# Performance work log

Measured on AMD Instinct MI355X. Metric: run time of the kernel, lower is better.

## Reference

```python
import math
import jax, jax.numpy as jnp
import numpy as np

D_MODEL = 768
D_CROSS = 768
D_HEAD = 64
N_HEADS = D_MODEL // D_HEAD  # 12
D_FF = D_MODEL * 3           # 2304
EPS = 1e-6
N_FREQ = D_HEAD // 8         # freqs per axis (3 axes -> theta dim 24, rotates first 48 of 64 dims)


def make_rope_freqs():
    # k-diffusion style geometric frequencies in [pi, 10*pi), one table shared per head
    n = N_HEADS * N_FREQ
    f = np.exp(np.linspace(math.log(math.pi), math.log(10.0 * math.pi), n + 1)[:-1])
    return jnp.asarray(f.reshape(N_FREQ, N_HEADS).T, dtype=jnp.float32)  # [nh, N_FREQ]

ROPE_FREQS = make_rope_freqs()


def rms_norm(x, scale):
    ms = jnp.mean(jnp.square(x), axis=-1, keepdims=True)
    return x * (scale * jax.lax.rsqrt(ms + EPS))


def cos_scale(q, k, scale):
    # cosine-sim QK rescale: unit-normalize q,k per head then multiply by sqrt(learned scale)
    s = jnp.sqrt(scale)[:, None, None]  # [nh,1,1]
    q = q * (s * jax.lax.rsqrt(jnp.sum(jnp.square(q), -1, keepdims=True) + EPS))
    k = k * (s * jax.lax.rsqrt(jnp.sum(jnp.square(k), -1, keepdims=True) + EPS))
    return q, k


def rope_theta(pos):
    # pos [b,l,3] -> theta [b,nh,l,3*N_FREQ]
    b, l, _ = pos.shape
    th = pos[..., None, :, None] * ROPE_FREQS[:, None, :]  # [b,l,nh,3,N_FREQ]
    th = th.reshape(b, l, N_HEADS, 3 * N_FREQ)
    return jnp.swapaxes(th, 1, 2)  # movedim(-2,-3)


def apply_rope(x, theta):
    d = theta.shape[-1]
    x1, x2, x3 = x[..., :d], x[..., d:2 * d], x[..., 2 * d:]
    c, s = jnp.cos(theta), jnp.sin(theta)
    return jnp.concatenate([x1 * c - x2 * s, x2 * c + x1 * s, x3], axis=-1)


def sdpa(q, k, v):
    # scale=1.0 (cosine-sim already scaled)
    a = jax.nn.softmax(jnp.einsum('bhqe,bhke->bhqk', q, k), axis=-1)
    return jnp.einsum('bhqk,bhke->bhqe', a, v)


def reference(x, pos, x_cross, pos_cross,
              sa_norm_scale, sa_wqkv, sa_scale, sa_wout,
              ca_norm_scale, ca_norm_cross_scale, ca_wq, ca_wkv, ca_scale, ca_wout,
              ff_norm_scale, ff_wup, ff_wdown):
    b, l, _ = x.shape
    lc = x_cross.shape[1]

    # --- self attention ---
    h = rms_norm(x, sa_norm_scale)
    qkv = (h @ sa_wqkv.T).reshape(b, l, 3, N_HEADS, D_HEAD).transpose(2, 0, 3, 1, 4)
    q, k, v = qkv[0], qkv[1], qkv[2]  # [b,nh,l,e]
    q, k = cos_scale(q, k, sa_scale)
    theta = rope_theta(pos)
    q = apply_rope(q, theta)
    k = apply_rope(k, theta)
    o = sdpa(q, k, v)
    o = jnp.swapaxes(o, 1, 2).reshape(b, l, D_MODEL)
    x = o @ sa_wout.T + x

    # --- cross attention ---
    h = rms_norm(x, ca_norm_scale)
    hc = rms_norm(x_cross, ca_norm_cross_scale)
    q = (h @ ca_wq.T).reshape(b, l, N_HEADS, D_HEAD).transpose(0, 2, 1, 3)
    kv = (hc @ ca_wkv.T).reshape(b, lc, 2, N_HEADS, D_HEAD).transpose(2, 0, 3, 1, 4)
    k, v = kv[0], kv[1]
    q, k = cos_scale(q, k, ca_scale)
    q = apply_rope(q, rope_theta(pos))
    k = apply_rope(k, rope_theta(pos_cross))
    o = sdpa(q, k, v)
    o = jnp.swapaxes(o, 1, 2).reshape(b, l, D_MODEL)
    x = o @ ca_wout.T + x

    # --- SwiGLU FFN ---
    u = rms_norm(x, ff_norm_scale) @ ff_wup.T  # [b,l,2*d_ff]
    a, g = jnp.split(u, 2, axis=-1)
    x = (a * jax.nn.silu(g)) @ ff_wdown.T + x
    return x


def setup_inputs() -> dict:
    key = jax.random.key(0)
    ks = jax.random.split(key, 16)
    B, L = 2, 2048

    def w(k, out_f, in_f):
        return jax.random.normal(k, (out_f, in_f), dtype=jnp.float32) * (1.0 / math.sqrt(in_f))

    return {
        'x': jax.random.normal(ks[0], (B, L, D_MODEL), dtype=jnp.float32),
        'pos': jax.random.uniform(ks[1], (B, L, 3), dtype=jnp.float32),
        'x_cross': jax.random.normal(ks[2], (B, L, D_CROSS), dtype=jnp.float32),
        'pos_cross': jax.random.uniform(ks[3], (B, L, 3), dtype=jnp.float32),
        'sa_norm_scale': jnp.ones((D_MODEL,), jnp.float32),
        'sa_wqkv': w(ks[4], 3 * D_MODEL, D_MODEL),
        'sa_scale': jnp.full((N_HEADS,), 10.0, jnp.float32),
        'sa_wout': w(ks[5], D_MODEL, D_MODEL) * 0.02,
        'ca_norm_scale': jnp.ones((D_MODEL,), jnp.float32),
        'ca_norm_cross_scale': jnp.ones((D_CROSS,), jnp.float32),
        'ca_wq': w(ks[6], D_MODEL, D_MODEL),
        'ca_wkv': w(ks[7], 2 * D_MODEL, D_CROSS),
        'ca_scale': jnp.full((N_HEADS,), 10.0, jnp.float32),
        'ca_wout': w(ks[8], D_MODEL, D_MODEL) * 0.02,
        'ff_norm_scale': jnp.ones((D_MODEL,), jnp.float32),
        'ff_wup': w(ks[9], 2 * D_FF, D_MODEL),
        'ff_wdown': w(ks[10], D_MODEL, D_FF) * 0.02,
    }
```

## Files before the change

### kernel.cpp

```cpp
#include <hip/hip_runtime.h>
#include <hip/hip_bf16.h>
#include <math.h>

typedef __hip_bfloat16 bf16;

#define B 2
#define L 2048
#define DM 768
#define NH 12
#define DH 64
#define DFF 2304
#define M_TOK (B * L)

typedef __attribute__((ext_vector_type(8))) short bfrag;
typedef __attribute__((ext_vector_type(4))) float ffrag;
typedef __attribute__((ext_vector_type(16))) float facc16;

__device__ __forceinline__ float waveSum(float v) {
#pragma unroll
  for (int o = 32; o > 0; o >>= 1) v += __shfl_down(v, o, 64);
  return v;
}

__device__ __forceinline__ void gld16(void* l, const void* g) {
  __builtin_amdgcn_global_load_lds((const __attribute__((address_space(1))) unsigned*)g,
                                   (__attribute__((address_space(3))) unsigned*)l, 16, 0, 0);
}

#define BAR1_N(N) do { asm volatile("s_waitcnt vmcnt(" #N ")" ::: "memory"); \
                       __builtin_amdgcn_s_barrier(); } while (0)
#define BAR2() do { asm volatile("s_waitcnt lgkmcnt(0)" ::: "memory"); \
                    __builtin_amdgcn_s_barrier(); } while (0)

#define ASW(row, chunk) (((row) << 6) + ((((chunk) ^ ((row)&7))) << 3))

__global__ void k_castall(const float* __restrict__ s0, const float* __restrict__ s1,
                          const float* __restrict__ s2, const float* __restrict__ s3,
                          const float* __restrict__ s4, const float* __restrict__ s5,
                          const float* __restrict__ s6, bf16* __restrict__ dst) {
  const size_t DM2 = (size_t)DM * DM;
  size_t u = ((size_t)blockIdx.x * 256 + threadIdx.x) * 4;
  if (u >= 17 * DM2) return;
  const float* src;
  size_t loc;
  if (u < 3 * DM2) { src = s0; loc = u; }
  else if (u < 4 * DM2) { src = s1; loc = u - 3 * DM2; }
  else if (u < 5 * DM2) { src = s2; loc = u - 4 * DM2; }
  else if (u < 7 * DM2) { src = s3; loc = u - 5 * DM2; }
  else if (u < 8 * DM2) { src = s4; loc = u - 7 * DM2; }
  else if (u < 14 * DM2) { src = s5; loc = u - 8 * DM2; }
  else { src = s6; loc = u - 14 * DM2; }
  float4 v = *(const float4*)&src[loc];
  bf16* d = dst + u;
  d[0] = __float2bfloat16(v.x);
  d[1] = __float2bfloat16(v.y);
  d[2] = __float2bfloat16(v.z);
  d[3] = __float2bfloat16(v.w);
}

__device__ __forceinline__ void rms_body(const float* __restrict__ in,
                                         const float* __restrict__ scale, int row, int t,
                                         bf16* __restrict__ out) {
  const float* r = in + (size_t)row * DM;
  float x0 = r[t], x1 = r[t + 256], x2 = r[t + 512];
  float ss = x0 * x0 + x1 * x1 + x2 * x2;
  ss = waveSum(ss);
  __shared__ float red[4];
  int w = t >> 6, ln = t & 63;
  if (ln == 0) red[w] = ss;
  __syncthreads();
  float tot = red[0] + red[1] + red[2] + red[3];
  float g = rsqrtf(tot / (float)DM + 1e-6f);
  bf16* o = out + (size_t)row * DM;
  o[t] = __float2bfloat16(x0 * g * scale[t]);
  o[t + 256] = __float2bfloat16(x1 * g * scale[t + 256]);
  o[t + 512] = __float2bfloat16(x2 * g * scale[t + 512]);
}

__global__ __launch_bounds__(256) void k_rmsnorm(const float* __restrict__ in,
                                                 const float* __restrict__ scale,
                                                 bf16* __restrict__ out) {
  rms_body(in, scale, blockIdx.x, threadIdx.x, out);
}

__global__ __launch_bounds__(256) void k_rmsnorm2(const float* __restrict__ in0,
                                                  const float* __restrict__ sc0,
                                                  bf16* __restrict__ out0,
                                                  const float* __restrict__ in1,
                                                  const float* __restrict__ sc1,
                                                  bf16* __restrict__ out1) {
  int row = blockIdx.x;
  if (row < M_TOK) rms_body(in0, sc0, row, threadIdx.x, out0);
  else rms_body(in1, sc1, row - M_TOK, threadIdx.x, out1);
}

template <int NT, int OBF>
__global__ __launch_bounds__(256) void k_gemm(const bf16* __restrict__ A,
                                              const bf16* __restrict__ W,
                                              float* __restrict__ C,
                                              bf16* __restrict__ Cb,
                                              const float* __restrict__ res,
                                              int M, int N, int K) {
  __shared__ __align__(16) bf16 As[2 * 128 * 64];
  __shared__ __align__(16) bf16 Bs[2 * NT * 64];
  const int t = threadIdx.x;
  const int w = t >> 6, lane = t & 63;
  const int m0 = blockIdx.y * 128, n0 = blockIdx.x * NT;
  const int quad = lane >> 4, l16 = lane & 15;
  constexpr int MI = (NT == 128) ? 4 : 2;
  const int wrow = (NT == 128) ? (w >> 1) * 64 : w * 32;
  const int wcol = (NT == 128) ? (w & 1) * 64 : 0;

  ffrag acc[MI][4];
#pragma unroll
  for (int i = 0; i < MI; i++)
#pragma unroll
    for (int j = 0; j < 4; j++) acc[i][j] = (ffrag){0.f, 0.f, 0.f, 0.f};

  const bf16 *pA[4], *pB[4];
  int lA[4], lB[4];
#pragma unroll
  for (int it = 0; it < 4; it++) {
    int lc = (w * 4 + it) * 64 + lane;
    int r = lc >> 3, c = lc & 7, kc = c ^ (r & 7);
    pA[it] = A + (size_t)(m0 + r) * K + kc * 8;
    lA[it] = lc * 8;
  }
  if (NT == 128) {
#pragma unroll
    for (int it = 0; it < 4; it++) {
      int lc = (w * 4 + it) * 64 + lane;
      int r = lc >> 3, c = lc & 7, kc = c ^ (r & 7);
      pB[it] = W + (size_t)(n0 + r) * K + kc * 8;
      lB[it] = lc * 8;
    }
  } else {
#pragma unroll
    for (int it = 0; it < 2; it++) {
      int lc = (w * 2 + it) * 64 + lane;
      int r = lc >> 3, c = lc & 7, kc = c ^ (r & 7);
      pB[it] = W + (size_t)(n0 + r) * K + kc * 8;
      lB[it] = lc * 8;
    }
  }
  auto stage = [&](int sel) {
#pragma unroll
    for (int it = 0; it < 4; it++) { gld16(&As[sel * 8192 + lA[it]], pA[it]); pA[it] += 64; }
    if (NT == 128) {
#pragma unroll
      for (int it = 0; it < 4; it++) { gld16(&Bs[sel * 8192 + lB[it]], pB[it]); pB[it] += 64; }
    } else {
#pragma unroll
      for (int it = 0; it < 2; it++) { gld16(&Bs[sel * 4096 + lB[it]], pB[it]); pB[it] += 64; }
    }
  };

  const int NK = K >> 6;
  stage(0);
  for (int kt = 0; kt < NK; kt++) {
    int cur = kt & 1;
    if (kt + 1 < NK) {
      stage(cur ^ 1);
      if constexpr (NT == 128) { BAR1_N(8); } else { BAR1_N(6); }
    } else {
      BAR1_N(0);
    }
    const bf16* Ab = As + cur * 8192;
    const bf16* Bb = Bs + cur * (NT == 128 ? 8192 : 4096);
#pragma unroll
    for (int s = 0; s < 2; s++) {
      bfrag af[MI], bfv[4];
#pragma unroll
      for (int i = 0; i < MI; i++)
        af[i] = *(const bfrag*)&Ab[ASW(wrow + i * 16 + l16, s * 4 + quad)];
#pragma unroll
      for (int j = 0; j < 4; j++)
        bfv[j] = *(const bfrag*)&Bb[ASW(wcol + j * 16 + l16, s * 4 + quad)];
#pragma unroll
      for (int i = 0; i < MI; i++)
#pragma unroll
        for (int j = 0; j < 4; j++)
          acc[i][j] = __builtin_amdgcn_mfma_f32_16x16x32_bf16(af[i], bfv[j], acc[i][j], 0, 0, 0);
    }
    BAR2();
  }
#pragma unroll
  for (int i = 0; i < MI; i++) {
    int mrow = m0 + wrow + i * 16 + quad * 4;
#pragma unroll
    for (int j = 0; j < 4; j++) {
      int ncol = n0 + wcol + j * 16 + l16;
#pragma unroll
      for (int r = 0; r < 4; r++) {
        float v = acc[i][j][r];
        size_t idx = (size_t)(mrow + r) * N + ncol;
        if (OBF) {
          Cb[idx] = __float2bfloat16(v);
        } else {
          if (res) v += res[idx];
          C[idx] = v;
        }
      }
    }
  }
}

__global__ __launch_bounds__(256) void k_ffup(const bf16* __restrict__ A,
                                              const bf16* __restrict__ Wup,
                                              bf16* __restrict__ Out) {
  __shared__ __align__(16) bf16 As[2 * 128 * 32];
  __shared__ __align__(16) bf16 Ba[2 * 64 * 32];
  __shared__ __align__(16) bf16 Bg[2 * 64 * 32];
  const int t = threadIdx.x, w = t >> 6, lane = t & 63;
  const int m0 = blockIdx.y * 128, n0 = blockIdx.x * 64;
  const int quad = lane >> 4, l16 = lane & 15;

  ffrag aa[2][4], ag[2][4];
#pragma unroll
  for (int i = 0; i < 2; i++)
#pragma unroll
    for (int j = 0; j < 4; j++) {
      aa[i][j] = (ffrag){0.f, 0.f, 0.f, 0.f};
      ag[i][j] = (ffrag){0.f, 0.f, 0.f, 0.f};
    }

  const bf16 *pA0, *pA1, *pBa, *pBg;
  int lA0, lA1, lBc;
  {
    int lc0 = (w * 2 + 0) * 64 + lane;
    int r0 = lc0 >> 2, kc0 = (lc0 & 3) ^ ((r0 >> 1) & 3);
    int lc1 = (w * 2 + 1) * 64 + lane;
    int r1 = lc1 >> 2, kc1 = (lc1 & 3) ^ ((r1 >> 1) & 3);
    pA0 = A + (size_t)(m0 + r0) * DM + kc0 * 8; lA0 = lc0 * 8;
    pA1 = A + (size_t)(m0 + r1) * DM + kc1 * 8; lA1 = lc1 * 8;
    int lc = w * 64 + lane;
    int r = lc >> 2, kc = (lc & 3) ^ ((r >> 1) & 3);
    pBa = Wup + (size_t)(n0 + r) * DM + kc * 8;
    pBg = Wup + (size_t)(DFF + n0 + r) * DM + kc * 8;
    lBc = lc * 8;
  }
  auto stage = [&](int sel) {
    gld16(&As[sel * 4096 + lA0], pA0); pA0 += 32;
    gld16(&As[sel * 4096 + lA1], pA1); pA1 += 32;
    gld16(&Ba[sel * 2048 + lBc], pBa); pBa += 32;
    gld16(&Bg[sel * 2048 + lBc], pBg); pBg += 32;
  };

  const int NK = DM / 32;
  stage(0);
  for (int kt = 0; kt < NK; kt++) {
    int cur = kt & 1;
    if (kt + 1 < NK) {
      stage(cur ^ 1);
      BAR1_N(4);
    } else {
      BAR1_N(0);
    }
    const bf16* Ab = As + cur * 4096;
    const bf16* Bab = Ba + cur * 2048;
    const bf16* Bgb = Bg + cur * 2048;
    bfrag af[2], ba[4], bg[4];
#pragma unroll
    for (int i = 0; i < 2; i++) {
      int r = w * 32 + i * 16 + l16;
      af[i] = *(const bfrag*)&Ab[r * 32 + (quad ^ ((r >> 1) & 3)) * 8];
    }
#pragma unroll
    for (int j = 0; j < 4; j++) {
      int r = j * 16 + l16;
      int sw = (quad ^ ((r >> 1) & 3)) * 8;
      ba[j] = *(const bfrag*)&Bab[r * 32 + sw];
      bg[j] = *(const bfrag*)&Bgb[r * 32 + sw];
    }
#pragma unroll
    for (int i = 0; i < 2; i++)
#pragma unroll
      for (int j = 0; j < 4; j++) {
        aa[i][j] = __builtin_amdgcn_mfma_f32_16x16x32_bf16(af[i], ba[j], aa[i][j], 0, 0, 0);
        ag[i][j] = __builtin_amdgcn_mfma_f32_16x16x32_bf16(af[i], bg[j], ag[i][j], 0, 0, 0);
      }
    BAR2();
  }
#pragma unroll
  for (int i = 0; i < 2; i++) {
    int mrow = m0 + w * 32 + i * 16 + quad * 4;
#pragma unroll
    for (int j = 0; j < 4; j++) {
      int ncol = n0 + j * 16 + l16;
#pragma unroll
      for (int r = 0; r < 4; r++) {
        float a = aa[i][j][r], g = ag[i][j][r];
        float v = a * g / (1.f + __expf(-g));
        Out[(size_t)(mrow + r) * DFF + ncol] = __float2bfloat16(v);
      }
    }
  }
}

__device__ __forceinline__ void rope8(const bf16* __restrict__ inp, const float* __restrict__ pos3,
                                      float s, float fr0, int k, int lane,
                                      bf16* __restrict__ outp) {
  bfrag v = *(const bfrag*)inp;
  float x[8];
#pragma unroll
  for (int i = 0; i < 8; i++) x[i] = __bfloat162float(__builtin_bit_cast(bf16, (short)v[i]));
  float ss = 0.f;
#pragma unroll
  for (int i = 0; i < 8; i++) ss += x[i] * x[i];
  ss += __shfl_xor(ss, 1, 64);
  ss += __shfl_xor(ss, 2, 64);
  ss += __shfl_xor(ss, 4, 64);
  float g = s * rsqrtf(ss + 1e-6f);
#pragma unroll
  for (int i = 0; i < 8; i++) x[i] *= g;
  int pk = k < 3 ? k + 3 : (k < 6 ? k - 3 : k);
  int psrc = (lane & 56) | pk;
  float other[8];
#pragma unroll
  for (int i = 0; i < 8; i++) other[i] = __shfl(x[i], psrc, 64);
  bfrag o;
  if (k < 6) {
    int c = k < 3 ? k : k - 3;
    float p = pos3[c];
    float fr = fr0;
    float sgn = k < 3 ? -1.f : 1.f;
#pragma unroll
    for (int i = 0; i < 8; i++) {
      float th = p * fr;
      fr *= 1.333521432163324f;
      float st = __sinf(th), ct = __cosf(th);
      o[i] = __builtin_bit_cast(short, __float2bfloat16(x[i] * ct + sgn * other[i] * st));
    }
  } else {
#pragma unroll
    for (int i = 0; i < 8; i++) o[i] = __builtin_bit_cast(short, __float2bfloat16(x[i]));
  }
  *(bfrag*)outp = o;
}

__global__ __launch_bounds__(256) void k_ropeqk(const bf16* __restrict__ inQ, int strQ, int offQ,
                                                const bf16* __restrict__ inK, int strK, int offK,
                                                const float* __restrict__ posQ,
                                                const float* __restrict__ posK,
                                                const float* __restrict__ scale,
                                                bf16* __restrict__ outQ, bf16* __restrict__ outK) {
  int wid = blockIdx.x * 4 + (threadIdx.x >> 6);
  int lane = threadIdx.x & 63;
  int k = lane & 7;
  int item = wid * 8 + (lane >> 3);
  int l = item % L;
  int bh = item / L;
  int h = bh % NH;
  int b = bh / NH;
  float s = sqrtf(scale[h]);
  float fr0 = __expf(1.14472988584940017f + (float)h * 0.023985261385354646f);
  size_t tokrow = (size_t)(b * L + l);
  rope8(inQ + tokrow * strQ + offQ + h * DH + k * 8, &posQ[tokrow * 3], s, fr0, k, lane,
        outQ + (size_t)item * DH + k * 8);
  rope8(inK + tokrow * strK + offK + h * DH + k * 8, &posK[tokrow * 3], s, fr0, k, lane,
        outK + (size_t)item * DH + k * 8);
}

__global__ __launch_bounds__(256) void k_vtrans(const bf16* __restrict__ in, int stride, int off,
                                                bf16* __restrict__ Vt) {
  __shared__ __align__(16) bf16 St[64 * 64];
  int lt = blockIdx.x & 31, bh = blockIdx.x >> 5;
  int h = bh % NH, b = bh / NH;
  int t = threadIdx.x;
#pragma unroll
  for (int pass = 0; pass < 2; pass++) {
    int cid = t + pass * 256;
    int r = cid >> 3, c = cid & 7;
    *(float4*)&St[ASW(r, c)] =
        *(const float4*)&in[(size_t)(b * L + lt * 64 + r) * stride + off + h * DH + c * 8];
  }
  __syncthreads();
  const short* Ss = (const short*)St;
#pragma unroll
  for (int pass = 0; pass < 2; pass++) {
    int cid = t + pass * 256;
    int d = cid >> 3, oc = cid & 7;
    bfrag tmp;
#pragma unroll
    for (int i = 0; i < 8; i++) {
      int p = oc * 8 + i;
      int tok = (p & ~12) | ((p & 4) << 1) | ((p & 8) >> 1);
      tmp[i] = Ss[(tok << 6) + ((((d >> 3) ^ (tok & 7))) << 3) + (d & 7)];
    }
    *(bfrag*)&Vt[((size_t)bh * DH + d) * L + lt * 64 + oc * 8] = tmp;
  }
}

__global__ __launch_bounds__(256) void k_attn_mfma(const bf16* __restrict__ Q,
                                                   const bf16* __restrict__ K,
                                                   const bf16* __restrict__ Vt,
                                                   const float* __restrict__ scale,
                                                   bf16* __restrict__ O) {
  __shared__ __align__(16) char smem[49152 + 512];
  bf16* Ks = (bf16*)smem;
  bf16* Vs = (bf16*)(smem + 24576);
  float* Oex = (float*)smem;
  float* Lred = (float*)(smem + 49152);
  int qt = blockIdx.x & 31, bh = blockIdx.x >> 5;
  int h = bh % NH, b = bh / NH;
  float smax = scale[h];
  float nsl2 = -smax * 1.442695040888963f;
  int t = threadIdx.x, w = t >> 6, lane = t & 63;
  int hh = lane >> 5, l32 = lane & 31;
  int qsub = w >> 1, ksub = w & 1;

  const bf16* kbase = K + (size_t)(bh * L) * DH;
  const bf16* vbase = Vt + (size_t)bh * DH * L;

  const bf16* qrow = Q + ((size_t)(bh * L) + qt * 64 + qsub * 32 + l32) * DH;
  bfrag qf[4];
#pragma unroll
  for (int c = 0; c < 4; c++) qf[c] = *(const bfrag*)&qrow[c * 16 + hh * 8];

  facc16 o0, o1;
#pragma unroll
  for (int i = 0; i < 16; i++) { o0[i] = 0.f; o1[i] = 0.f; }
  float l_run = 0.f;

  const bf16 *kg0, *kg1, *vg0, *vg1;
  int lk0, lk1;
  {
    int r0 = w * 8 + (lane >> 3);
    int kc0 = (lane & 7) ^ (r0 & 7);
    int r1 = r0 + 32;
    int kc1 = (lane & 7) ^ (r1 & 7);
    kg0 = kbase + (size_t)r0 * DH + kc0 * 8;
    kg1 = kbase + (size_t)r1 * DH + kc1 * 8;
    vg0 = vbase + (size_t)r0 * L + kc0 * 8;
    vg1 = vbase + (size_t)r1 * L + kc1 * 8;
    lk0 = (w * 8) * 64 + lane * 8;
    lk1 = (w * 8 + 32) * 64 + lane * 8;
  }
  auto stageKV = [&](int sel) {
    gld16(&Ks[sel * 4096 + lk0], kg0); kg0 += 64 * DH;
    gld16(&Ks[sel * 4096 + lk1], kg1); kg1 += 64 * DH;
    gld16(&Vs[sel * 4096 + lk0], vg0); vg0 += 64;
    gld16(&Vs[sel * 4096 + lk1], vg1); vg1 += 64;
  };

  stageKV(0);
  stageKV(1);
  int cur = 0;
  for (int kt = 0; kt < 32; kt++) {
    if (kt < 31) { BAR1_N(4); } else { BAR1_N(0); }
    if (kt + 2 < 32) {
      int nb = cur + 2; if (nb >= 3) nb -= 3;
      stageKV(nb);
    }
    const bf16* Kb = Ks + cur * 4096;
    const bf16* Vb = Vs + cur * 4096;
    facc16 s;
#pragma unroll
    for (int i = 0; i < 16; i++) s[i] = 0.f;
#pragma unroll
    for (int c = 0; c < 4; c++) {
      bfrag kf = *(const bfrag*)&Kb[ASW(ksub * 32 + l32, c * 2 + hh)];
      s = __builtin_amdgcn_mfma_f32_32x32x16_bf16(kf, qf[c], s, 0, 0, 0);
    }
    float pv[16];
#pragma unroll
    for (int reg = 0; reg < 16; reg++) {
      float p = __builtin_amdgcn_exp2f(__builtin_fmaf(s[reg], 1.442695040888963f, nsl2));
      l_run += p;
      pv[reg] = p;
    }
    bfrag pf0, pf1;
#pragma unroll
    for (int j = 0; j < 8; j++) {
      pf0[j] = __builtin_bit_cast(short, __float2bfloat16(pv[j]));
      pf1[j] = __builtin_bit_cast(short, __float2bfloat16(pv[8 + j]));
    }
    {
      bfrag vf;
      vf = *(const bfrag*)&Vb[ASW(l32, ksub * 4 + hh)];
      o0 = __builtin_amdgcn_mfma_f32_32x32x16_bf16(pf0, vf, o0, 0, 0, 0);
      vf = *(const bfrag*)&Vb[ASW(l32, ksub * 4 + 2 + hh)];
      o0 = __builtin_amdgcn_mfma_f32_32x32x16_bf16(pf1, vf, o0, 0, 0, 0);
      vf = *(const bfrag*)&Vb[ASW(32 + l32, ksub * 4 + hh)];
      o1 = __builtin_amdgcn_mfma_f32_32x32x16_bf16(pf0, vf, o1, 0, 0, 0);
      vf = *(const bfrag*)&Vb[ASW(32 + l32, ksub * 4 + 2 + hh)];
      o1 = __builtin_amdgcn_mfma_f32_32x32x16_bf16(pf1, vf, o1, 0, 0, 0);
    }
    cur = (cur == 2) ? 0 : cur + 1;
  }
  l_run += __shfl_xor(l_run, 32, 64);
  __syncthreads();
  {
    int gd = (ksub ^ 1) * 32 + l32;
#pragma unroll
    for (int reg = 0; reg < 16; reg++) {
      int row = (reg & 3) + 8 * (reg >> 2) + 4 * hh;
      float gv = ksub ? o0[reg] : o1[reg];
      Oex[(size_t)(qsub * 32 + row) * 64 + gd] = gv;
    }
  }
  if (lane < 32) Lred[ksub * 64 + qsub * 32 + lane] = l_run;
  __syncthreads();
  {
    int d = ksub * 32 + l32;
#pragma unroll
    for (int reg = 0; reg < 16; reg++) {
      int row = (reg & 3) + 8 * (reg >> 2) + 4 * hh;
      int qg2 = qsub * 32 + row;
      float ltot = Lred[qg2] + Lred[64 + qg2];
      float keep = ksub ? o1[reg] : o0[reg];
      float v = (keep + Oex[(size_t)qg2 * 64 + d]) / ltot;
      O[(((size_t)(b * L) + qt * 64 + qg2) * NH + h) * DH + d] = __float2bfloat16(v);
    }
  }
}

extern "C" void kernel_launch(void* const* d_in, const int* in_sizes, int n_in,
                              void* d_out, int out_size, void* d_ws, size_t ws_size,
                              hipStream_t stream) {
  const float* x = (const float*)d_in[0];
  const float* pos = (const float*)d_in[1];
  const float* x_cross = (const float*)d_in[2];
  const float* pos_cross = (const float*)d_in[3];
  const float* sa_norm_scale = (const float*)d_in[4];
  const float* sa_wqkv = (const float*)d_in[5];
  const float* sa_scale = (const float*)d_in[6];
  const float* sa_wout = (const float*)d_in[7];
  const float* ca_norm_scale = (const float*)d_in[8];
  const float* ca_norm_cross_scale = (const float*)d_in[9];
  const float* ca_wq = (const float*)d_in[10];
  const float* ca_wkv = (const float*)d_in[11];
  const float* ca_scale = (const float*)d_in[12];
  const float* ca_wout = (const float*)d_in[13];
  const float* ff_norm_scale = (const float*)d_in[14];
  const float* ff_wup = (const float*)d_in[15];
  const float* ff_wdown = (const float*)d_in[16];
  float* out = (float*)d_out;

  float* ws = (float*)d_ws;
  const size_t S = (size_t)M_TOK * DM;
  float* xbuf = ws;
  bf16* b16 = (bf16*)(ws + S);
  bf16* qkvb = b16;
  bf16* qb = b16 + 3 * S;
  bf16* kb = b16 + 4 * S;
  bf16* vtb = b16 + 5 * S;
  bf16* hb = b16 + 6 * S;
  bf16* hcb = b16 + 7 * S;
  bf16* obb = b16 + 8 * S;
  bf16* wqkvb = b16 + 9 * S;
  bf16* woutb = wqkvb + (size_t)3 * DM * DM;
  bf16* wqb = woutb + (size_t)DM * DM;
  bf16* wkvb = wqb + (size_t)DM * DM;
  bf16* wout2b = wkvb + (size_t)2 * DM * DM;
  bf16* wupb = wout2b + (size_t)DM * DM;
  bf16* wdownb = wupb + (size_t)2 * DFF * DM;
  bf16* ffb = qkvb;

  const int ropeGrid = B * NH * L / 32;
  const int attnGrid = B * NH * (L / 64);
  const int vtGrid = B * NH * (L / 64);
  const size_t DM2 = (size_t)DM * DM;
  const int castGrid = (int)((17 * DM2 / 4 + 255) / 256);

  k_castall<<<castGrid, 256, 0, stream>>>(sa_wqkv, sa_wout, ca_wq, ca_wkv, ca_wout, ff_wup,
                                          ff_wdown, wqkvb);

  k_rmsnorm2<<<2 * M_TOK, 256, 0, stream>>>(x, sa_norm_scale, hb, x_cross, ca_norm_cross_scale,
                                            hcb);

  k_gemm<128, 1><<<dim3(3 * DM / 128, M_TOK / 128), 256, 0, stream>>>(
      hb, wqkvb, nullptr, qkvb, nullptr, M_TOK, 3 * DM, DM);
  k_ropeqk<<<ropeGrid, 256, 0, stream>>>(qkvb, 3 * DM, 0, qkvb, 3 * DM, DM, pos, pos, sa_scale,
                                         qb, kb);
  k_vtrans<<<vtGrid, 256, 0, stream>>>(qkvb, 3 * DM, 2 * DM, vtb);
  k_attn_mfma<<<attnGrid, 256, 0, stream>>>(qb, kb, vtb, sa_scale, obb);
  k_gemm<64, 0><<<dim3(DM / 64, M_TOK / 128), 256, 0, stream>>>(
      obb, woutb, xbuf, nullptr, x, M_TOK, DM, DM);

  k_rmsnorm<<<M_TOK, 256, 0, stream>>>(xbuf, ca_norm_scale, hb);
  k_gemm<64, 1><<<dim3(DM / 64, M_TOK / 128), 256, 0, stream>>>(
      hb, wqb, nullptr, qkvb, nullptr, M_TOK, DM, DM);
  k_gemm<128, 1><<<dim3(2 * DM / 128, M_TOK / 128), 256, 0, stream>>>(
      hcb, wkvb, nullptr, qkvb + S, nullptr, M_TOK, 2 * DM, DM);
  k_ropeqk<<<ropeGrid, 256, 0, stream>>>(qkvb, DM, 0, qkvb + S, 2 * DM, 0, pos, pos_cross,
                                         ca_scale, qb, kb);
  k_vtrans<<<vtGrid, 256, 0, stream>>>(qkvb + S, 2 * DM, DM, vtb);
  k_attn_mfma<<<attnGrid, 256, 0, stream>>>(qb, kb, vtb, ca_scale, obb);
  k_gemm<64, 0><<<dim3(DM / 64, M_TOK / 128), 256, 0, stream>>>(
      obb, wout2b, xbuf, nullptr, xbuf, M_TOK, DM, DM);

  k_rmsnorm<<<M_TOK, 256, 0, stream>>>(xbuf, ff_norm_scale, hb);
  k_ffup<<<dim3(DFF / 64, M_TOK / 128), 256, 0, stream>>>(hb, wupb, ffb);
  k_gemm<64, 0><<<dim3(DM / 64, M_TOK / 128), 256, 0, stream>>>(
      ffb, wdownb, out, nullptr, xbuf, M_TOK, DM, DFF);
}
```

Baseline: 431.3 us.

## Process two 64-query subtiles per attention block to reuse staged K/V

Each attention workgroup now owns 128 query rows as two 64-row subtiles sharing the same shared-memory K/V tiles. V fragments are loaded from LDS once per key tile and used for both subtiles, and the grid is halved. This cuts global K/V traffic and LDS fragment reads per query. The cost is higher register pressure from four output accumulators plus two sets of Q fragments, and fewer blocks (384 on 256 CUs), which can leave CUs unevenly loaded.

```diff
diff --git a/kernel.cpp b/kernel.cpp
--- a/kernel.cpp
+++ b/kernel.cpp
@@ -401,7 +401,7 @@
   bf16* Vs = (bf16*)(smem + 24576);
   float* Oex = (float*)smem;
   float* Lred = (float*)(smem + 49152);
-  int qt = blockIdx.x & 31, bh = blockIdx.x >> 5;
+  int qt = blockIdx.x & 15, bh = blockIdx.x >> 4;
   int h = bh % NH, b = bh / NH;
   float smax = scale[h];
   float nsl2 = -smax * 1.442695040888963f;
@@ -412,15 +412,19 @@
   const bf16* kbase = K + (size_t)(bh * L) * DH;
   const bf16* vbase = Vt + (size_t)bh * DH * L;
 
-  const bf16* qrow = Q + ((size_t)(bh * L) + qt * 64 + qsub * 32 + l32) * DH;
-  bfrag qf[4];
-#pragma unroll
-  for (int c = 0; c < 4; c++) qf[c] = *(const bfrag*)&qrow[c * 16 + hh * 8];
-
-  facc16 o0, o1;
-#pragma unroll
-  for (int i = 0; i < 16; i++) { o0[i] = 0.f; o1[i] = 0.f; }
-  float l_run = 0.f;
+  const bf16* qrowA = Q + ((size_t)(bh * L) + qt * 128 + qsub * 32 + l32) * DH;
+  const bf16* qrowB = qrowA + (size_t)64 * DH;
+  bfrag qfA[4], qfB[4];
+#pragma unroll
+  for (int c = 0; c < 4; c++) {
+    qfA[c] = *(const bfrag*)&qrowA[c * 16 + hh * 8];
+    qfB[c] = *(const bfrag*)&qrowB[c * 16 + hh * 8];
+  }
+
+  facc16 o0A, o1A, o0B, o1B;
+#pragma unroll
+  for (int i = 0; i < 16; i++) { o0A[i] = 0.f; o1A[i] = 0.f; o0B[i] = 0.f; o1B[i] = 0.f; }
+  float lA = 0.f, lB = 0.f;
 
   const bf16 *kg0, *kg1, *vg0, *vg1;
   int lk0, lk1;
@@ -454,63 +458,76 @@
     }
     const bf16* Kb = Ks + cur * 4096;
     const bf16* Vb = Vs + cur * 4096;
-    facc16 s;
-#pragma unroll
-    for (int i = 0; i < 16; i++) s[i] = 0.f;
-#pragma unroll
-    for (int c = 0; c < 4; c++) {
-      bfrag kf = *(const bfrag*)&Kb[ASW(ksub * 32 + l32, c * 2 + hh)];
-      s = __builtin_amdgcn_mfma_f32_32x32x16_bf16(kf, qf[c], s, 0, 0, 0);
-    }
-    float pv[16];
-#pragma unroll
-    for (int reg = 0; reg < 16; reg++) {
-      float p = __builtin_amdgcn_exp2f(__builtin_fmaf(s[reg], 1.442695040888963f, nsl2));
-      l_run += p;
-      pv[reg] = p;
-    }
-    bfrag pf0, pf1;
-#pragma unroll
-    for (int j = 0; j < 8; j++) {
-      pf0[j] = __builtin_bit_cast(short, __float2bfloat16(pv[j]));
-      pf1[j] = __builtin_bit_cast(short, __float2bfloat16(pv[8 + j]));
-    }
+    bfrag vf0 = *(const bfrag*)&Vb[ASW(l32, ksub * 4 + hh)];
+    bfrag vf1 = *(const bfrag*)&Vb[ASW(l32, ksub * 4 + 2 + hh)];
+    bfrag vf2 = *(const bfrag*)&Vb[ASW(32 + l32, ksub * 4 + hh)];
+    bfrag vf3 = *(const bfrag*)&Vb[ASW(32 + l32, ksub * 4 + 2 + hh)];
+#pragma unroll
+    for (int sub = 0; sub < 2; sub++) {
+      const bfrag* qf = sub ? qfB : qfA;
+      facc16 s;
+#pragma unroll
+      for (int i = 0; i < 16; i++) s[i] = 0.f;
+#pragma unroll
+      for (int c = 0; c < 4; c++) {
+        bfrag kf = *(const bfrag*)&Kb[ASW(ksub * 32 + l32, c * 2 + hh)];
+        s = __builtin_amdgcn_mfma_f32_32x32x16_bf16(kf, qf[c], s, 0, 0, 0);
+      }
+      float pv[16];
+      float lp0 = 0.f, lp1 = 0.f;
+#pragma unroll
+      for (int reg = 0; reg < 16; reg += 2) {
+        float p0 = __builtin_amdgcn_exp2f(__builtin_fmaf(s[reg], 1.442695040888963f, nsl2));
+        float p1 = __builtin_amdgcn_exp2f(__builtin_fmaf(s[reg + 1], 1.442695040888963f, nsl2));
+        lp0 += p0; lp1 += p1;
+        pv[reg] = p0; pv[reg + 1] = p1;
+      }
+      if (sub) lB += lp0 + lp1; else lA += lp0 + lp1;
+      bfrag pf0, pf1;
+#pragma unroll
+      for (int j = 0; j < 8; j++) {
+        pf0[j] = __builtin_bit_cast(short, __float2bfloat16(pv[j]));
+        pf1[j] = __builtin_bit_cast(short, __float2bfloat16(pv[8 + j]));
+      }
+      facc16& e0 = sub ? o0B : o0A;
+      facc16& e1 = sub ? o1B : o1A;
+      e0 = __builtin_amdgcn_mfma_f32_32x32x16_bf16(pf0, vf0, e0, 0, 0, 0);
+      e0 = __builtin_amdgcn_mfma_f32_32x32x16_bf16(pf1, vf1, e0, 0, 0, 0);
+      e1 = __builtin_amdgcn_mfma_f32_32x32x16_bf16(pf0, vf2, e1, 0, 0, 0);
+      e1 = __builtin_amdgcn_mfma_f32_32x32x16_bf16(pf1, vf3, e1, 0, 0, 0);
+    }
+    cur = (cur == 2) ? 0 : cur + 1;
+  }
+#pragma unroll
+  for (int sub = 0; sub < 2; sub++) {
+    facc16& e0 = sub ? o0B : o0A;
+    facc16& e1 = sub ? o1B : o1A;
+    float l_run = sub ? lB : lA;
+    l_run += __shfl_xor(l_run, 32, 64);
+    __syncthreads();
     {
-      bfrag vf;
-      vf = *(const bfrag*)&Vb[ASW(l32, ksub * 4 + hh)];
-      o0 = __builtin_amdgcn_mfma_f32_32x32x16_bf16(pf0, vf, o0, 0, 0, 0);
-      vf = *(const bfrag*)&Vb[ASW(l32, ksub * 4 + 2 + hh)];
-      o0 = __builtin_amdgcn_mfma_f32_32x32x16_bf16(pf1, vf, o0, 0, 0, 0);
-      vf = *(const bfrag*)&Vb[ASW(32 + l32, ksub * 4 + hh)];
-      o1 = __builtin_amdgcn_mfma_f32_32x32x16_bf16(pf0, vf, o1, 0, 0, 0);
-      vf = *(const bfrag*)&Vb[ASW(32 + l32, ksub * 4 + 2 + hh)];
-      o1 = __builtin_amdgcn_mfma_f32_32x32x16_bf16(pf1, vf, o1, 0, 0, 0);
-    }
-    cur = (cur == 2) ? 0 : cur + 1;
-  }
-  l_run += __shfl_xor(l_run, 32, 64);
-  __syncthreads();
-  {
-    int gd = (ksub ^ 1) * 32 + l32;
-#pragma unroll
-    for (int reg = 0; reg < 16; reg++) {
-      int row = (reg & 3) + 8 * (reg >> 2) + 4 * hh;
-      float gv = ksub ? o0[reg] : o1[reg];
-      Oex[(size_t)(qsub * 32 + row) * 64 + gd] = gv;
-    }
-  }
-  if (lane < 32) Lred[ksub * 64 + qsub * 32 + lane] = l_run;
-  __syncthreads();
-  {
-    int d = ksub * 32 + l32;
-#pragma unroll
-    for (int reg = 0; reg < 16; reg++) {
-      int row = (reg & 3) + 8 * (reg >> 2) + 4 * hh;
-      int qg2 = qsub * 32 + row;
-      float ltot = Lred[qg2] + Lred[64 + qg2];
-      float keep = ksub ? o1[reg] : o0[reg];
-      float v = (keep + Oex[(size_t)qg2 * 64 + d]) / ltot;
-      O[(((size_t)(b * L) + qt * 64 + qg2) * NH + h) * DH + d] = __float2bfloat16(v);
+      int gd = (ksub ^ 1) * 32 + l32;
+#pragma unroll
+      for (int reg = 0; reg < 16; reg++) {
+        int row = (reg & 3) + 8 * (reg >> 2) + 4 * hh;
+        float gv = ksub ? e0[reg] : e1[reg];
+        Oex[(size_t)(qsub * 32 + row) * 64 + gd] = gv;
+      }
+    }
+    if (lane < 32) Lred[ksub * 64 + qsub * 32 + lane] = l_run;
+    __syncthreads();
+    {
+      int d = ksub * 32 + l32;
+#pragma unroll
+      for (int reg = 0; reg < 16; reg++) {
+        int row = (reg & 3) + 8 * (reg >> 2) + 4 * hh;
+        int qg2 = qsub * 32 + row;
+        float ltot = Lred[qg2] + Lred[64 + qg2];
+        float keep = ksub ? e1[reg] : e0[reg];
+        float v = (keep + Oex[(size_t)qg2 * 64 + d]) / ltot;
+        O[(((size_t)(b * L) + qt * 128 + sub * 64 + qg2) * NH + h) * DH + d] =
+            __float2bfloat16(v);
+      }
     }
   }
 }
@@ -558,7 +575,7 @@
   bf16* ffb = qkvb;
 
   const int ropeGrid = B * NH * L / 32;
-  const int attnGrid = B * NH * (L / 64);
+  const int attnGrid = B * NH * (L / 128);
   const int vtGrid = B * NH * (L / 64);
   const size_t DM2 = (size_t)DM * DM;
   const int castGrid = (int)((17 * DM2 / 4 + 255) / 256);
```

Measured after the change: 448.4 us. 3.9% more time.
